# Optimization experiments

Measured on AMD Instinct MI355X. Metric: run time of the kernel, lower is better.

The kernel has to match this reference:

```python
import jax, jax.numpy as jnp
import numpy as np

P = 16      # patch size
DM = 512    # d_model
DI = 1024   # d_inner = expand * d_model
N = 16      # d_state
K = 4       # d_conv
DR = 32     # dt_rank = ceil(d_model/16)
NL = 8      # n_layers
NC = 1000   # num_classes


def _ln(x, w, b):
    m = x.mean(-1, keepdims=True)
    v = x.var(-1, keepdims=True)
    return (x - m) * jax.lax.rsqrt(v + 1e-5) * w + b


def _fpad(x, wl, wr, ht, hb):
    # torch F.pad(x, (wl, wr, ht, hb)) with possibly negative (crop) values, NCHW
    x = jnp.pad(x, ((0, 0), (0, 0), (max(ht, 0), max(hb, 0)), (max(wl, 0), max(wr, 0))))
    return x[:, :, -min(ht, 0):x.shape[2] + min(hb, 0), -min(wl, 0):x.shape[3] + min(wr, 0)]


def _mamba(x, in_w, conv_w, conv_b, xproj_w, dt_w, dt_b, A_log, Dp, out_w):
    # standard mamba_ssm Mamba layer; weights stored (in, out)
    B, L, _ = x.shape
    xz = x @ in_w                         # (B, L, 2*DI)
    xpart, z = xz[..., :DI], xz[..., DI:]
    # depthwise causal conv1d, kernel K, padding K-1 then truncate to L
    xc = jnp.pad(xpart.transpose(0, 2, 1), ((0, 0), (0, 0), (K - 1, 0)))  # (B, DI, L+K-1)
    conv = conv_b[None, :, None] + sum(conv_w[None, :, k, None] * xc[:, :, k:k + L] for k in range(K))
    u = jax.nn.silu(conv).transpose(0, 2, 1)    # (B, L, DI)
    dbc = u @ xproj_w                           # (B, L, DR + 2N)
    dt = jax.nn.softplus(dbc[..., :DR] @ dt_w + dt_b)  # (B, L, DI)
    Bm, Cm = dbc[..., DR:DR + N], dbc[..., DR + N:]
    A = -jnp.exp(A_log)                         # (DI, N)
    dA = jnp.exp(dt[..., None] * A)             # (B, L, DI, N)
    dBu = (dt * u)[..., None] * Bm[:, :, None, :]

    def step(h, inp):
        dA_t, dBu_t, C_t = inp
        h = dA_t * h + dBu_t                    # (B, DI, N)
        return h, jnp.einsum('bdn,bn->bd', h, C_t)

    h0 = jnp.zeros((B, DI, N), x.dtype)
    _, ys = jax.lax.scan(step, h0, (dA.transpose(1, 0, 2, 3), dBu.transpose(1, 0, 2, 3), Cm.transpose(1, 0, 2)))
    y = ys.transpose(1, 0, 2) + u * Dp          # (B, L, DI)
    return (y * jax.nn.silu(z)) @ out_w         # (B, L, DM)


def reference(img, patch_ln_w, patch_ln_b, patch_w, patch_b, pos_emb, cls_tok,
              ln_w, ln_b, in_w, conv_w, conv_b, xproj_w, dt_w, dt_b, A_log, D, out_w,
              head_ln_w, head_ln_b, head_w, head_b):
    shifts = ((1, -1, 0, 0), (-1, 1, 0, 0), (0, 0, 1, -1), (0, 0, -1, 1))
    x5 = jnp.concatenate([img] + [_fpad(img, *s) for s in shifts], axis=1)  # (B, 15, H, W)
    Bn, C, H, W = x5.shape
    # 'b c (h p1) (w p2) -> b (h w) (p1 p2 c)'
    x = x5.reshape(Bn, C, H // P, P, W // P, P).transpose(0, 2, 4, 3, 5, 1).reshape(Bn, (H // P) * (W // P), P * P * C)
    x = _ln(x, patch_ln_w, patch_ln_b) @ patch_w + patch_b  # (B, n, DM)
    n = x.shape[1]
    x = jnp.concatenate([x, jnp.broadcast_to(cls_tok, (Bn, 1, DM))], axis=1)  # cls appended at END
    x = x + pos_emb[:, :n + 1]
    for i in range(NL):
        y = _ln(x, ln_w[i], ln_b[i])
        x = x + _mamba(y, in_w[i], conv_w[i], conv_b[i], xproj_w[i], dt_w[i], dt_b[i], A_log[i], D[i], out_w[i])
    x = x[:, -1]  # pool='cls' -> last token
    return _ln(x, head_ln_w, head_ln_b) @ head_w + head_b


def setup_inputs() -> dict:
    key = jax.random.key(0)
    ks = jax.random.split(key, 12)
    B = 8
    PD = P * P * 15  # 3840
    rn = lambda k, shape, scale=1.0: jax.random.normal(k, shape, jnp.float32) * scale
    return {
        "img": rn(ks[0], (B, 3, 224, 224)),
        "patch_ln_w": jnp.ones((PD,), jnp.float32), "patch_ln_b": jnp.zeros((PD,), jnp.float32),
        "patch_w": rn(ks[1], (PD, DM), PD ** -0.5), "patch_b": jnp.zeros((DM,), jnp.float32),
        "pos_emb": rn(ks[2], (1, 197, DM), 0.02),
        "cls_tok": rn(ks[3], (1, 1, DM), 0.02),
        "ln_w": jnp.ones((NL, DM), jnp.float32), "ln_b": jnp.zeros((NL, DM), jnp.float32),
        "in_w": rn(ks[4], (NL, DM, 2 * DI), DM ** -0.5),
        "conv_w": rn(ks[5], (NL, DI, K), K ** -0.5),
        "conv_b": jnp.zeros((NL, DI), jnp.float32),
        "xproj_w": rn(ks[6], (NL, DI, DR + 2 * N), DI ** -0.5),
        "dt_w": rn(ks[7], (NL, DR, DI), DR ** -0.5),
        "dt_b": rn(ks[8], (NL, DI), 0.1) - 4.0,  # softplus -> small positive dt
        "A_log": jnp.log(jnp.broadcast_to(jnp.arange(1.0, N + 1.0, dtype=jnp.float32), (NL, DI, N))),
        "D": jnp.ones((NL, DI), jnp.float32),
        "out_w": rn(ks[9], (NL, DI, DM), DI ** -0.5),
        "head_ln_w": jnp.ones((DM,), jnp.float32), "head_ln_b": jnp.zeros((DM,), jnp.float32),
        "head_w": rn(ks[10], (DM, NC), DM ** -0.5), "head_b": jnp.zeros((NC,), jnp.float32),
    }
```

## Files before the change

kernel.cpp:

```cpp
#include <hip/hip_runtime.h>
#include <hip/hip_fp16.h>
#include <math.h>

#define BATCH   8
#define LSEQ    197
#define LPAD    200
#define NPATCH  196
#define NPTOK   (BATCH * NPATCH)
#define NTOK    (BATCH * LSEQ)
#define MPAD    1664
#define DMODEL  512
#define DINNER  1024
#define NSTATE  16
#define DRANK   32
#define NLAYER  8
#define NCLS    1000
#define PDIM    3840

typedef _Float16 f16x8 __attribute__((ext_vector_type(8)));
typedef float    f32x4 __attribute__((ext_vector_type(4)));
typedef unsigned short us8 __attribute__((ext_vector_type(8)));

__device__ __forceinline__ float f_rcp(float x) { return __builtin_amdgcn_rcpf(x); }
__device__ __forceinline__ float sp_silu(float x) { return x * f_rcp(1.0f + __expf(-x)); }
__device__ __forceinline__ float sp_softplus(float x) {
    return x > 20.0f ? x : __logf(1.0f + __expf(x));
}

template <int N>
__device__ __forceinline__ void vm_wait() {
    if constexpr (N == 0) asm volatile("s_waitcnt vmcnt(0)" ::: "memory");
    else if constexpr (N == 4) asm volatile("s_waitcnt vmcnt(4)" ::: "memory");
    else if constexpr (N == 6) asm volatile("s_waitcnt vmcnt(6)" ::: "memory");
    else if constexpr (N == 8) asm volatile("s_waitcnt vmcnt(8)" ::: "memory");
}

#define DPP_ROW_SHR_STEP(P, NB, CTRL)                                          \
    {                                                                          \
        float t_[NB];                                                          \
        _Pragma("unroll")                                                      \
        for (int i_ = 0; i_ < NB; ++i_)                                        \
            t_[i_] = __int_as_float(__builtin_amdgcn_update_dpp(               \
                0, __float_as_int(P[i_]), CTRL, 0xF, 0xF, true));              \
        _Pragma("unroll")                                                      \
        for (int i_ = 0; i_ < NB; ++i_) P[i_] += t_[i_];                       \
    }

template <int NB>
__device__ __forceinline__ void row_sum16v(float* p) {
    DPP_ROW_SHR_STEP(p, NB, 0x111);
    DPP_ROW_SHR_STEP(p, NB, 0x112);
    DPP_ROW_SHR_STEP(p, NB, 0x114);
    DPP_ROW_SHR_STEP(p, NB, 0x118);
}

__device__ __forceinline__ void store_f16(char* __restrict__ Hb,
                                          int row, int k, int K, float v) {
    size_t byte = (size_t)row * (size_t)(K * 2) +
                  (size_t)(((unsigned)(k * 2)) ^ (unsigned)((row & 7) << 4));
    *(__half*)(Hb + byte) = __float2half_rn(v);
}

__device__ __forceinline__ void store_f16x4(char* __restrict__ Hb,
                                            int row, int k4, int K, float4 v) {
    size_t byte = (size_t)row * (size_t)(K * 2) +
                  (size_t)(((unsigned)(k4 * 2)) ^ (unsigned)((row & 7) << 4));
    *(ushort4*)(Hb + byte) = make_ushort4(
        __half_as_ushort(__float2half_rn(v.x)), __half_as_ushort(__float2half_rn(v.y)),
        __half_as_ushort(__float2half_rn(v.z)), __half_as_ushort(__float2half_rn(v.w)));
}

__device__ __forceinline__ float2 block_reduce2(float a, float b, float* lds) {
#pragma unroll
    for (int off = 32; off > 0; off >>= 1) {
        a += __shfl_down(a, off);
        b += __shfl_down(b, off);
    }
    int lane = threadIdx.x & 63, w = threadIdx.x >> 6;
    if (lane == 0) { lds[w] = a; lds[4 + w] = b; }
    __syncthreads();
    float sa = lds[0] + lds[1] + lds[2] + lds[3];
    float sb = lds[4] + lds[5] + lds[6] + lds[7];
    return make_float2(sa, sb);
}

__global__ __launch_bounds__(256) void k_patch_ln(
    const float* __restrict__ img, const float* __restrict__ lnw,
    const float* __restrict__ lnb, char* __restrict__ Xph) {
    __shared__ float vals[PDIM];
    __shared__ float red[8];
    int tok = blockIdx.x;
    int b = tok / NPATCH, p = tok % NPATCH;
    int gy = p / 14, gx = p % 14;
    int tid = threadIdx.x;
    int py = tid >> 4, px = tid & 15;
    int h0 = gy * 16 + py, w0 = gx * 16 + px;
    const int dh[5] = {0, 0, 0, -1, 1};
    const int dw[5] = {0, -1, 1, 0, 0};
    float s = 0.f, ss = 0.f;
#pragma unroll
    for (int c = 0; c < 15; ++c) {
        int g = c / 3, ch = c % 3;
        int h = h0 + dh[g], w = w0 + dw[g];
        float v = 0.f;
        if ((unsigned)h < 224u && (unsigned)w < 224u)
            v = img[((b * 3 + ch) * 224 + h) * 224 + w];
        vals[tid * 15 + c] = v;
        s += v; ss += v * v;
    }
    float2 t2 = block_reduce2(s, ss, red);
    float mean = t2.x * (1.0f / PDIM);
    float var  = t2.y * (1.0f / PDIM) - mean * mean;
    float rstd = 1.0f / sqrtf(var + 1e-5f);
    for (int j = 0; j < 15; ++j) {
        int e = tid + j * 256;
        float v = (vals[e] - mean) * rstd * lnw[e] + lnb[e];
        store_f16(Xph, tok, e, PDIM, v);
    }
}

__global__ __launch_bounds__(256) void k_ln(
    const float* __restrict__ x, const float* __restrict__ w,
    const float* __restrict__ b, char* __restrict__ yh) {
    __shared__ float red[8];
    int t = blockIdx.x, tid = threadIdx.x;
    const float* xr = x + (size_t)t * DMODEL;
    float v0 = xr[tid], v1 = xr[tid + 256];
    float2 t2 = block_reduce2(v0 + v1, v0 * v0 + v1 * v1, red);
    float mean = t2.x * (1.0f / DMODEL);
    float var  = t2.y * (1.0f / DMODEL) - mean * mean;
    float rstd = 1.0f / sqrtf(var + 1e-5f);
    store_f16(yh, t, tid,       DMODEL, (v0 - mean) * rstd * w[tid]       + b[tid]);
    store_f16(yh, t, tid + 256, DMODEL, (v1 - mean) * rstd * w[tid + 256] + b[tid + 256]);
}

__global__ __launch_bounds__(256) void k_red_ln(
    const float* __restrict__ part, float* __restrict__ xtok,
    const float* __restrict__ w, const float* __restrict__ b,
    char* __restrict__ yh) {
    __shared__ float red[8];
    int t = blockIdx.x, tid = threadIdx.x;
    size_t base = (size_t)t * DMODEL;
    float v0 = xtok[base + tid], v1 = xtok[base + tid + 256];
#pragma unroll
    for (int k = 0; k < 4; ++k) {
        v0 += part[(size_t)k * (NTOK * DMODEL) + base + tid];
        v1 += part[(size_t)k * (NTOK * DMODEL) + base + tid + 256];
    }
    xtok[base + tid] = v0;
    xtok[base + tid + 256] = v1;
    float2 t2 = block_reduce2(v0 + v1, v0 * v0 + v1 * v1, red);
    float mean = t2.x * (1.0f / DMODEL);
    float var  = t2.y * (1.0f / DMODEL) - mean * mean;
    float rstd = 1.0f / sqrtf(var + 1e-5f);
    store_f16(yh, t, tid,       DMODEL, (v0 - mean) * rstd * w[tid]       + b[tid]);
    store_f16(yh, t, tid + 256, DMODEL, (v1 - mean) * rstd * w[tid + 256] + b[tid + 256]);
}

__global__ __launch_bounds__(256) void k_wT(
    const float* __restrict__ W, char* __restrict__ Th,
    int Ks, int Ns, size_t wStride, size_t tByteStride) {
    __shared__ float t[32][33];
    int z = blockIdx.z;
    const float* Wz = W + (size_t)z * wStride;
    char* ThZ = Th + (size_t)z * tByteStride;
    int n0 = blockIdx.x * 32, k0 = blockIdx.y * 32;
    int tx = threadIdx.x, ty = threadIdx.y;
#pragma unroll
    for (int r = 0; r < 4; ++r) {
        int k = k0 + ty + r * 8, n = n0 + tx;
        t[tx][ty + r * 8] = (n < Ns) ? Wz[(size_t)k * Ns + n] : 0.f;
    }
    __syncthreads();
#pragma unroll
    for (int r = 0; r < 4; ++r) {
        int n = n0 + ty + r * 8, k = k0 + tx;
        float v = t[ty + r * 8][tx];
        size_t byte = (size_t)n * (size_t)(Ks * 2) +
                      (size_t)(((unsigned)(k * 2)) ^ (unsigned)((n & 7) << 4));
        *(__half*)(ThZ + byte) = __float2half_rn(v);
    }
}

template <int TM, int TN, bool F16OUT>
__global__ __launch_bounds__(256, 3) void k_gemm(
    const char* __restrict__ Ah, const char* __restrict__ Bh,
    float* __restrict__ C, unsigned short* __restrict__ C16,
    int M, int N, int K, int kchunk, long partStride) {
    constexpr int MW = TM / 2, NW = TN / 2;
    constexpr int FM = MW / 16, FN = NW / 16;
    constexpr int CPW = (TM + TN) / 32;
    __shared__ __half L[2][(TM + TN) * 64];
    const int tid = threadIdx.x, w = tid >> 6, lane = tid & 63;

    const int GX = gridDim.x, GY = gridDim.y;
    const int nwg = GX * GY * gridDim.z;
    const int orig = blockIdx.x + GX * (blockIdx.y + GY * blockIdx.z);
    const int q = nwg >> 3, r = nwg & 7, xcd = orig & 7, pos = orig >> 3;
    const int wrk = (xcd < r ? xcd * (q + 1) : r * (q + 1) + (xcd - r) * q) + pos;
    const int bm = wrk % GY;
    const int t1 = wrk / GY;
    const int bn = t1 % GX, bz = t1 / GX;

    const int m0 = bm * TM, n0 = bn * TN;
    const int kbeg = bz * kchunk;
    int kend = kbeg + kchunk; if (kend > K) kend = K;
    C += (size_t)bz * (size_t)partStride;
    const size_t K2 = (size_t)K * 2;
    const int srLane = lane >> 3;
    const int scol = (lane & 7) * 16;

    f32x4 acc[FM][FN];
#pragma unroll
    for (int i = 0; i < FM; ++i)
#pragma unroll
        for (int j = 0; j < FN; ++j) acc[i][j] = (f32x4)(0.f);

    auto STAGE = [&](int buf, int k0) {
#pragma unroll
        for (int i = 0; i < CPW; ++i) {
            int cid = w * CPW + i;
            bool isA = cid < TM / 8;
            int lr = (isA ? cid : cid - TM / 8) * 8;
            size_t go = (size_t)((isA ? m0 : n0) + lr + srLane) * K2 +
                        (size_t)k0 * 2 + scol;
            const char* src = isA ? Ah : Bh;
            int ldsOff = (isA ? 0 : TM * 64) + lr * 64;
            __builtin_amdgcn_global_load_lds(
                (const __attribute__((address_space(1))) void*)(src + go),
                (__attribute__((address_space(3))) void*)&L[buf][ldsOff], 16, 0, 0);
        }
    };

    const int wm = w >> 1, wn = w & 1;
    const int g = lane >> 4, rr = lane & 15;
    const int nk = (kend - kbeg + 63) / 64;

    STAGE(0, kbeg);

    for (int t = 0; t < nk; ++t) {
        int cur = t & 1;
        if (t + 1 < nk) {
            STAGE(cur ^ 1, kbeg + (t + 1) * 64);
            vm_wait<CPW>();
        } else {
            vm_wait<0>();
        }
        __builtin_amdgcn_s_barrier();
        const char* Lb = (const char*)L[cur];
#pragma unroll
        for (int kk = 0; kk < 2; ++kk) {
            f16x8 af[FM], bf[FN];
#pragma unroll
            for (int mf = 0; mf < FM; ++mf) {
                int row = wm * MW + mf * 16 + rr;
                int off = row * 128 + ((kk * 64 + g * 16) ^ ((row & 7) << 4));
                af[mf] = *(const f16x8*)(Lb + off);
            }
#pragma unroll
            for (int nf = 0; nf < FN; ++nf) {
                int row = wn * NW + nf * 16 + rr;
                int off = TM * 128 + row * 128 +
                          ((kk * 64 + g * 16) ^ ((row & 7) << 4));
                bf[nf] = *(const f16x8*)(Lb + off);
            }
#pragma unroll
            for (int mf = 0; mf < FM; ++mf)
#pragma unroll
                for (int nf = 0; nf < FN; ++nf)
                    acc[mf][nf] = __builtin_amdgcn_mfma_f32_16x16x32_f16(
                        af[mf], bf[nf], acc[mf][nf], 0, 0, 0);
        }
        __builtin_amdgcn_s_barrier();
    }

#pragma unroll
    for (int mf = 0; mf < FM; ++mf)
#pragma unroll
        for (int nf = 0; nf < FN; ++nf)
#pragma unroll
            for (int e = 0; e < 4; ++e) {
                int gm = m0 + wm * MW + mf * 16 + g * 4 + e;
                int gn = n0 + wn * NW + nf * 16 + rr;
                if (gm < M && gn < N) {
                    if (F16OUT)
                        C16[(size_t)gm * N + gn] =
                            __half_as_ushort(__float2half_rn(acc[mf][nf][e]));
                    else
                        C[(size_t)gm * N + gn] = acc[mf][nf][e];
                }
            }
}

template <int SK, bool ACC>
__global__ __launch_bounds__(256) void k_reduce(
    const float* __restrict__ part, float* __restrict__ out, int total, int stride) {
    int i = blockIdx.x * 256 + threadIdx.x;
    if (i >= total) return;
    float s = 0.f;
#pragma unroll
    for (int k = 0; k < SK; ++k) s += part[(size_t)k * stride + i];
    out[i] = ACC ? out[i] + s : s;
}

__global__ __launch_bounds__(256) void k_assemble(
    const float* __restrict__ Pe, const float* __restrict__ patch_b,
    const float* __restrict__ cls, const float* __restrict__ pos,
    float* __restrict__ xtok) {
    int idx = blockIdx.x * 256 + threadIdx.x;
    if (idx >= NTOK * DMODEL) return;
    int d = idx % DMODEL;
    int t = (idx / DMODEL) % LSEQ;
    int b = idx / (DMODEL * LSEQ);
    float v = (t < NPATCH) ? (Pe[((size_t)b * NPATCH + t) * DMODEL + d] + patch_b[d])
                           : cls[d];
    xtok[idx] = v + pos[t * DMODEL + d];
}

__global__ __launch_bounds__(256) void k_conv(
    const unsigned short* __restrict__ xzH, const float* __restrict__ cw,
    const float* __restrict__ cb, char* __restrict__ uh) {
    int idx = blockIdx.x * 256 + threadIdx.x;
    if (idx >= NTOK * (DINNER / 4)) return;
    int dq = idx & (DINNER / 4 - 1);
    int t  = idx / (DINNER / 4);
    int l  = t % LSEQ;
    int d  = dq * 4;
    float4 w0 = *(const float4*)&cw[(d + 0) * 4];
    float4 w1 = *(const float4*)&cw[(d + 1) * 4];
    float4 w2 = *(const float4*)&cw[(d + 2) * 4];
    float4 w3 = *(const float4*)&cw[(d + 3) * 4];
    float4 acc = *(const float4*)&cb[d];
#pragma unroll
    for (int j = 0; j < 4; ++j) {
        int ls = l - 3 + j;
        if (ls >= 0) {
            union { ushort4 v; __half h[4]; } xu;
            xu.v = *(const ushort4*)&xzH[(size_t)(t - 3 + j) * (2 * DINNER) + d];
            acc.x += (&w0.x)[j] * __half2float(xu.h[0]);
            acc.y += (&w1.x)[j] * __half2float(xu.h[1]);
            acc.z += (&w2.x)[j] * __half2float(xu.h[2]);
            acc.w += (&w3.x)[j] * __half2float(xu.h[3]);
        }
    }
    float4 uv = make_float4(sp_silu(acc.x), sp_silu(acc.y),
                            sp_silu(acc.z), sp_silu(acc.w));
    store_f16x4(uh, t, d, DINNER, uv);
}

__global__ __launch_bounds__(256) void k_scan2(
    const char* __restrict__ uH, const float* __restrict__ dbc,
    const float* __restrict__ dtw, const float* __restrict__ dtb,
    const float* __restrict__ Alog, const float* __restrict__ Dp,
    const unsigned short* __restrict__ xzH, char* __restrict__ gh) {
    __shared__ float uS[LPAD * 16];
    __shared__ float dS[LPAD * 16];
    __shared__ float bS[LPAD * 16];
    __shared__ float cS[LPAD * 16];
    __shared__ float wS[DRANK * 16];
    const int tid = threadIdx.x;
    const int b = blockIdx.y, d0 = blockIdx.x * 16;

    for (int i = tid; i < DRANK * 16; i += 256)
        wS[i] = dtw[(size_t)(i >> 4) * DINNER + d0 + (i & 15)];
    __syncthreads();

    for (int i = tid; i < LPAD * 2; i += 256) {
        int l = i >> 1, jj = i & 1;
        float* dst = &uS[l * 16 + jj * 8];
        if (l >= LSEQ) {
#pragma unroll
            for (int e = 0; e < 8; ++e) dst[e] = 0.f;
            continue;
        }
        int t = b * LSEQ + l;
        size_t byte = (size_t)t * (DINNER * 2) +
                      (size_t)(((unsigned)(d0 * 2 + jj * 16)) ^ (unsigned)((t & 7) << 4));
        union { us8 v; __half h[8]; } uu;
        uu.v = *(const us8*)(uH + byte);
#pragma unroll
        for (int e = 0; e < 8; ++e) dst[e] = __half2float(uu.h[e]);
    }

    const float* dbcB = dbc + ((size_t)b * LSEQ) * 64;
    for (int i = tid; i < LPAD * 4; i += 256) {
        int l = i >> 2, j = (i & 3) << 2;
        if (l >= LSEQ) {
            float4 z = make_float4(0.f, 0.f, 0.f, 0.f);
            *(float4*)&dS[l * 16 + j] = z;
            *(float4*)&bS[l * 16 + j] = z;
            *(float4*)&cS[l * 16 + j] = z;
            continue;
        }
        *(float4*)&bS[l * 16 + j] = *(const float4*)&dbcB[(size_t)l * 64 + DRANK + j];
        *(float4*)&cS[l * 16 + j] = *(const float4*)&dbcB[(size_t)l * 64 + DRANK + 16 + j];
        float4 acc = *(const float4*)&dtb[d0 + j];
#pragma unroll
        for (int kq = 0; kq < DRANK / 4; ++kq) {
            float4 r4 = *(const float4*)&dbcB[(size_t)l * 64 + kq * 4];
#pragma unroll
            for (int m = 0; m < 4; ++m) {
                float rv = (&r4.x)[m];
                float4 w4 = *(const float4*)&wS[(kq * 4 + m) * 16 + j];
                acc.x += rv * w4.x; acc.y += rv * w4.y;
                acc.z += rv * w4.z; acc.w += rv * w4.w;
            }
        }
        dS[l * 16 + j + 0] = sp_softplus(acc.x);
        dS[l * 16 + j + 1] = sp_softplus(acc.y);
        dS[l * 16 + j + 2] = sp_softplus(acc.z);
        dS[l * 16 + j + 3] = sp_softplus(acc.w);
    }
    const int n = tid & 15, dsub = tid >> 4;
    const int d = d0 + dsub;
    const float A  = -__expf(Alog[d * NSTATE + n]);
    const float Dv = Dp[d];
    __syncthreads();

    float hn = 0.f;
    float dtc[8], uvc[8], Bnc[8], Cnc[8];
#pragma unroll
    for (int i = 0; i < 8; ++i) {
        int o = i * 16;
        dtc[i] = dS[o + dsub]; uvc[i] = uS[o + dsub];
        Bnc[i] = bS[o + n];    Cnc[i] = cS[o + n];
    }
    for (int lb = 0; lb < LPAD; lb += 8) {
        float dtN[8], uvN[8], BnN[8], CnN[8];
        if (lb + 8 < LPAD) {
#pragma unroll
            for (int i = 0; i < 8; ++i) {
                int o = (lb + 8 + i) * 16;
                dtN[i] = dS[o + dsub]; uvN[i] = uS[o + dsub];
                BnN[i] = bS[o + n];    CnN[i] = cS[o + n];
            }
        } else {
#pragma unroll
            for (int i = 0; i < 8; ++i) { dtN[i] = uvN[i] = BnN[i] = CnN[i] = 0.f; }
        }
        float a8[8], b8[8], p8[8];
#pragma unroll
        for (int i = 0; i < 8; ++i) {
            a8[i] = __expf(dtc[i] * A);
            b8[i] = dtc[i] * uvc[i] * Bnc[i];
        }
#pragma unroll
        for (int i = 0; i < 8; ++i) {
            hn = a8[i] * hn + b8[i];
            p8[i] = hn * Cnc[i];
        }
        row_sum16v<8>(p8);
#pragma unroll
        for (int i = 0; i < 8; ++i)
            if (n == 15) dS[(lb + i) * 16 + dsub] = p8[i] + uvc[i] * Dv;
#pragma unroll
        for (int i = 0; i < 8; ++i) {
            dtc[i] = dtN[i]; uvc[i] = uvN[i]; Bnc[i] = BnN[i]; Cnc[i] = CnN[i];
        }
    }
    __syncthreads();

    for (int i = tid; i < LSEQ * 4; i += 256) {
        int l = i >> 2, j = (i & 3) << 2;
        int t = b * LSEQ + l;
        union { ushort4 v; __half h[4]; } zu;
        zu.v = *(const ushort4*)&xzH[(size_t)t * (2 * DINNER) + DINNER + d0 + j];
        float4 g4 = make_float4(
            dS[l * 16 + j + 0] * sp_silu(__half2float(zu.h[0])),
            dS[l * 16 + j + 1] * sp_silu(__half2float(zu.h[1])),
            dS[l * 16 + j + 2] * sp_silu(__half2float(zu.h[2])),
            dS[l * 16 + j + 3] * sp_silu(__half2float(zu.h[3])));
        store_f16x4(gh, t, d0 + j, DINNER, g4);
    }
}

__global__ __launch_bounds__(256) void k_head_ln(
    const float* __restrict__ part, const float* __restrict__ xtok,
    const float* __restrict__ lnw, const float* __restrict__ lnb,
    float* __restrict__ xr) {
    __shared__ float red[8];
    int b = blockIdx.x, tid = threadIdx.x;
    size_t base = ((size_t)(b * LSEQ + NPATCH)) * DMODEL;
    float v0 = xtok[base + tid], v1 = xtok[base + tid + 256];
#pragma unroll
    for (int k = 0; k < 4; ++k) {
        v0 += part[(size_t)k * (NTOK * DMODEL) + base + tid];
        v1 += part[(size_t)k * (NTOK * DMODEL) + base + tid + 256];
    }
    float2 t2 = block_reduce2(v0 + v1, v0 * v0 + v1 * v1, red);
    float mean = t2.x * (1.0f / DMODEL);
    float var  = t2.y * (1.0f / DMODEL) - mean * mean;
    float rstd = 1.0f / sqrtf(var + 1e-5f);
    xr[b * DMODEL + tid]       = (v0 - mean) * rstd * lnw[tid] + lnb[tid];
    xr[b * DMODEL + tid + 256] = (v1 - mean) * rstd * lnw[tid + 256] + lnb[tid + 256];
}

__global__ __launch_bounds__(256) void k_head_fc(
    const float* __restrict__ xr, const float* __restrict__ hw,
    float* __restrict__ hpart) {
    __shared__ float xs[64];
    int tid = threadIdx.x;
    int c = blockIdx.x * 256 + tid;
    int b = blockIdx.y, ks = blockIdx.z;
    if (tid < 64) xs[tid] = xr[b * DMODEL + ks * 64 + tid];
    __syncthreads();
    if (c >= NCLS) return;
    float acc = 0.f;
#pragma unroll 8
    for (int k = 0; k < 64; ++k) acc += xs[k] * hw[(size_t)(ks * 64 + k) * NCLS + c];
    hpart[(size_t)(ks * BATCH + b) * NCLS + c] = acc;
}

__global__ __launch_bounds__(256) void k_head_red(
    const float* __restrict__ hpart, const float* __restrict__ hb,
    float* __restrict__ out) {
    int i = blockIdx.x * 256 + threadIdx.x;
    if (i >= BATCH * NCLS) return;
    int b = i / NCLS, c = i % NCLS;
    float s = hb[c];
#pragma unroll
    for (int ks = 0; ks < 8; ++ks) s += hpart[(size_t)(ks * BATCH + b) * NCLS + c];
    out[i] = s;
}

extern "C" void kernel_launch(void* const* d_in, const int* in_sizes, int n_in,
                              void* d_out, int out_size, void* d_ws, size_t ws_size,
                              hipStream_t stream) {
    const float* img     = (const float*)d_in[0];
    const float* plnw    = (const float*)d_in[1];
    const float* plnb    = (const float*)d_in[2];
    const float* patch_w = (const float*)d_in[3];
    const float* patch_b = (const float*)d_in[4];
    const float* pos     = (const float*)d_in[5];
    const float* cls     = (const float*)d_in[6];
    const float* ln_w    = (const float*)d_in[7];
    const float* ln_b    = (const float*)d_in[8];
    const float* in_w    = (const float*)d_in[9];
    const float* conv_w  = (const float*)d_in[10];
    const float* conv_b  = (const float*)d_in[11];
    const float* xproj   = (const float*)d_in[12];
    const float* dt_w    = (const float*)d_in[13];
    const float* dt_b    = (const float*)d_in[14];
    const float* A_log   = (const float*)d_in[15];
    const float* Dp      = (const float*)d_in[16];
    const float* out_w   = (const float*)d_in[17];
    const float* hlnw    = (const float*)d_in[18];
    const float* hlnb    = (const float*)d_in[19];
    const float* head_w  = (const float*)d_in[20];
    const float* head_b  = (const float*)d_in[21];
    float* out = (float*)d_out;

    char* p = (char*)d_ws;
    auto alloc = [&](size_t bytes) { char* r = p; p += (bytes + 255) & ~(size_t)255; return r; };
    float* xtok = (float*)alloc((size_t)NTOK * DMODEL * 4);
    unsigned short* xzH = (unsigned short*)alloc((size_t)NTOK * 2 * DINNER * 2);
    float* dbc  = (float*)alloc((size_t)NTOK * 64 * 4);
    float* Pe   = (float*)alloc((size_t)NPTOK * DMODEL * 4);
    float* part = (float*)alloc((size_t)4 * NTOK * DMODEL * 4);
    float* xr   = (float*)alloc((size_t)BATCH * DMODEL * 4);
    float* hpart= (float*)alloc((size_t)8 * BATCH * NCLS * 4);
    char* ylnH = alloc((size_t)MPAD * DMODEL * 2);
    char* uH   = alloc((size_t)MPAD * DINNER * 2);
    char* gH   = alloc((size_t)MPAD * DINNER * 2);
    char* XpH  = alloc((size_t)MPAD * PDIM * 2);
    char* inTH  = alloc((size_t)NLAYER * 2 * DINNER * DMODEL * 2);
    char* outTH = alloc((size_t)NLAYER * DMODEL * DINNER * 2);
    char* patTH = alloc((size_t)DMODEL * PDIM * 2);
    char* xprTH = alloc((size_t)NLAYER * 128 * DINNER * 2);

    const size_t IN_T_B  = (size_t)2 * DINNER * DMODEL * 2;
    const size_t OUT_T_B = (size_t)DMODEL * DINNER * 2;
    const size_t XPR_T_B = (size_t)128 * DINNER * 2;

    k_wT<<<dim3(2 * DINNER / 32, DMODEL / 32, NLAYER), dim3(32, 8), 0, stream>>>(
        in_w, inTH, DMODEL, 2 * DINNER, (size_t)DMODEL * 2 * DINNER, IN_T_B);
    k_wT<<<dim3(DMODEL / 32, DINNER / 32, NLAYER), dim3(32, 8), 0, stream>>>(
        out_w, outTH, DINNER, DMODEL, (size_t)DINNER * DMODEL, OUT_T_B);
    k_wT<<<dim3(DMODEL / 32, PDIM / 32, 1), dim3(32, 8), 0, stream>>>(
        patch_w, patTH, PDIM, DMODEL, 0, 0);
    k_wT<<<dim3(128 / 32, DINNER / 32, NLAYER), dim3(32, 8), 0, stream>>>(
        xproj, xprTH, DINNER, 64, (size_t)DINNER * 64, XPR_T_B);

    k_patch_ln<<<NPTOK, 256, 0, stream>>>(img, plnw, plnb, XpH);
    k_gemm<64, 128, false><<<dim3(4, 25, 4), 256, 0, stream>>>(
        XpH, patTH, part, nullptr, NPTOK, DMODEL, PDIM, 960, (long)NPTOK * DMODEL);
    k_reduce<4, false><<<(NPTOK * DMODEL + 255) / 256, 256, 0, stream>>>(
        part, Pe, NPTOK * DMODEL, NPTOK * DMODEL);
    k_assemble<<<(NTOK * DMODEL + 255) / 256, 256, 0, stream>>>(Pe, patch_b, cls, pos, xtok);

    for (int i = 0; i < NLAYER; ++i) {
        if (i == 0) {
            k_ln<<<NTOK, 256, 0, stream>>>(xtok, ln_w, ln_b, ylnH);
        } else {
            k_red_ln<<<NTOK, 256, 0, stream>>>(part, xtok, ln_w + i * DMODEL,
                                               ln_b + i * DMODEL, ylnH);
        }
        k_gemm<64, 128, true><<<dim3(16, 25, 1), 256, 0, stream>>>(
            ylnH, inTH + i * IN_T_B, nullptr, xzH, NTOK, 2 * DINNER, DMODEL, DMODEL, 0);
        k_conv<<<(NTOK * (DINNER / 4) + 255) / 256, 256, 0, stream>>>(
            xzH, conv_w + (size_t)i * DINNER * 4, conv_b + (size_t)i * DINNER, uH);
        k_gemm<64, 64, false><<<dim3(1, 25, 8), 256, 0, stream>>>(
            uH, xprTH + i * XPR_T_B, part, nullptr, NTOK, 64, DINNER, 128, (long)NTOK * 64);
        k_reduce<8, false><<<(NTOK * 64 + 255) / 256, 256, 0, stream>>>(
            part, dbc, NTOK * 64, NTOK * 64);
        k_scan2<<<dim3(DINNER / 16, BATCH), 256, 0, stream>>>(
            uH, dbc, dt_w + (size_t)i * DRANK * DINNER, dt_b + (size_t)i * DINNER,
            A_log + (size_t)i * DINNER * NSTATE, Dp + (size_t)i * DINNER,
            xzH, gH);
        k_gemm<64, 128, false><<<dim3(4, 25, 4), 256, 0, stream>>>(
            gH, outTH + i * OUT_T_B, part, nullptr, NTOK, DMODEL, DINNER, 256,
            (long)NTOK * DMODEL);
    }

    k_head_ln<<<BATCH, 256, 0, stream>>>(part, xtok, hlnw, hlnb, xr);
    k_head_fc<<<dim3(4, BATCH, 8), 256, 0, stream>>>(xr, head_w, hpart);
    k_head_red<<<(BATCH * NCLS + 255) / 256, 256, 0, stream>>>(hpart, head_b, out);
}
```

Before: 547.6 us.

## Triple-buffer GEMM staging, fuse patch reduce, reduce split-K, prefetch gate in scan

```diff
diff --git a/kernel.cpp b/kernel.cpp
--- a/kernel.cpp
+++ b/kernel.cpp
@@ -29,10 +29,11 @@
 
 template <int N>
 __device__ __forceinline__ void vm_wait() {
-    if constexpr (N == 0) asm volatile("s_waitcnt vmcnt(0)" ::: "memory");
-    else if constexpr (N == 4) asm volatile("s_waitcnt vmcnt(4)" ::: "memory");
-    else if constexpr (N == 6) asm volatile("s_waitcnt vmcnt(6)" ::: "memory");
-    else if constexpr (N == 8) asm volatile("s_waitcnt vmcnt(8)" ::: "memory");
+    if constexpr (N == 0)       asm volatile("s_waitcnt vmcnt(0)" ::: "memory");
+    else if constexpr (N == 4)  asm volatile("s_waitcnt vmcnt(4)" ::: "memory");
+    else if constexpr (N == 6)  asm volatile("s_waitcnt vmcnt(6)" ::: "memory");
+    else if constexpr (N == 8)  asm volatile("s_waitcnt vmcnt(8)" ::: "memory");
+    else if constexpr (N == 12) asm volatile("s_waitcnt vmcnt(12)" ::: "memory");
 }
 
 #define DPP_ROW_SHR_STEP(P, NB, CTRL)                                          \
@@ -143,7 +144,7 @@
     size_t base = (size_t)t * DMODEL;
     float v0 = xtok[base + tid], v1 = xtok[base + tid + 256];
 #pragma unroll
-    for (int k = 0; k < 4; ++k) {
+    for (int k = 0; k < 2; ++k) {
         v0 += part[(size_t)k * (NTOK * DMODEL) + base + tid];
         v1 += part[(size_t)k * (NTOK * DMODEL) + base + tid + 256];
     }
@@ -183,14 +184,14 @@
 }
 
 template <int TM, int TN, bool F16OUT>
-__global__ __launch_bounds__(256, 3) void k_gemm(
+__global__ __launch_bounds__(256, 2) void k_gemm(
     const char* __restrict__ Ah, const char* __restrict__ Bh,
     float* __restrict__ C, unsigned short* __restrict__ C16,
     int M, int N, int K, int kchunk, long partStride) {
     constexpr int MW = TM / 2, NW = TN / 2;
     constexpr int FM = MW / 16, FN = NW / 16;
     constexpr int CPW = (TM + TN) / 32;
-    __shared__ __half L[2][(TM + TN) * 64];
+    __shared__ __half L[3][(TM + TN) * 64];
     const int tid = threadIdx.x, w = tid >> 6, lane = tid & 63;
 
     const int GX = gridDim.x, GY = gridDim.y;
@@ -237,17 +238,19 @@
     const int nk = (kend - kbeg + 63) / 64;
 
     STAGE(0, kbeg);
+    if (1 < nk) STAGE(1, kbeg + 64);
 
     for (int t = 0; t < nk; ++t) {
-        int cur = t & 1;
-        if (t + 1 < nk) {
-            STAGE(cur ^ 1, kbeg + (t + 1) * 64);
+        if (t + 2 < nk) {
+            STAGE((t + 2) % 3, kbeg + (t + 2) * 64);
+            vm_wait<2 * CPW>();
+        } else if (t + 1 < nk) {
             vm_wait<CPW>();
         } else {
             vm_wait<0>();
         }
         __builtin_amdgcn_s_barrier();
-        const char* Lb = (const char*)L[cur];
+        const char* Lb = (const char*)L[t % 3];
 #pragma unroll
         for (int kk = 0; kk < 2; ++kk) {
             f16x8 af[FM], bf[FN];
@@ -303,8 +306,8 @@
     out[i] = ACC ? out[i] + s : s;
 }
 
-__global__ __launch_bounds__(256) void k_assemble(
-    const float* __restrict__ Pe, const float* __restrict__ patch_b,
+__global__ __launch_bounds__(256) void k_patch_asm(
+    const float* __restrict__ part, const float* __restrict__ patch_b,
     const float* __restrict__ cls, const float* __restrict__ pos,
     float* __restrict__ xtok) {
     int idx = blockIdx.x * 256 + threadIdx.x;
@@ -312,8 +315,16 @@
     int d = idx % DMODEL;
     int t = (idx / DMODEL) % LSEQ;
     int b = idx / (DMODEL * LSEQ);
-    float v = (t < NPATCH) ? (Pe[((size_t)b * NPATCH + t) * DMODEL + d] + patch_b[d])
-                           : cls[d];
+    float v;
+    if (t < NPATCH) {
+        size_t pi = ((size_t)(b * NPATCH + t)) * DMODEL + d;
+        float s = patch_b[d];
+#pragma unroll
+        for (int k = 0; k < 4; ++k) s += part[(size_t)k * (NPTOK * DMODEL) + pi];
+        v = s;
+    } else {
+        v = cls[d];
+    }
     xtok[idx] = v + pos[t * DMODEL + d];
 }
 
@@ -415,6 +426,17 @@
     const int d = d0 + dsub;
     const float A  = -__expf(Alog[d * NSTATE + n]);
     const float Dv = Dp[d];
+
+    ushort4 zreg[4];
+#pragma unroll
+    for (int it = 0; it < 4; ++it) {
+        int i = tid + it * 256;
+        if (i < LSEQ * 4) {
+            int l = i >> 2, j = (i & 3) << 2;
+            int t = b * LSEQ + l;
+            zreg[it] = *(const ushort4*)&xzH[(size_t)t * (2 * DINNER) + DINNER + d0 + j];
+        }
+    }
     __syncthreads();
 
     float hn = 0.f;
@@ -460,17 +482,21 @@
     }
     __syncthreads();
 
-    for (int i = tid; i < LSEQ * 4; i += 256) {
-        int l = i >> 2, j = (i & 3) << 2;
-        int t = b * LSEQ + l;
-        union { ushort4 v; __half h[4]; } zu;
-        zu.v = *(const ushort4*)&xzH[(size_t)t * (2 * DINNER) + DINNER + d0 + j];
-        float4 g4 = make_float4(
-            dS[l * 16 + j + 0] * sp_silu(__half2float(zu.h[0])),
-            dS[l * 16 + j + 1] * sp_silu(__half2float(zu.h[1])),
-            dS[l * 16 + j + 2] * sp_silu(__half2float(zu.h[2])),
-            dS[l * 16 + j + 3] * sp_silu(__half2float(zu.h[3])));
-        store_f16x4(gh, t, d0 + j, DINNER, g4);
+#pragma unroll
+    for (int it = 0; it < 4; ++it) {
+        int i = tid + it * 256;
+        if (i < LSEQ * 4) {
+            int l = i >> 2, j = (i & 3) << 2;
+            int t = b * LSEQ + l;
+            union { ushort4 v; __half h[4]; } zu;
+            zu.v = zreg[it];
+            float4 g4 = make_float4(
+                dS[l * 16 + j + 0] * sp_silu(__half2float(zu.h[0])),
+                dS[l * 16 + j + 1] * sp_silu(__half2float(zu.h[1])),
+                dS[l * 16 + j + 2] * sp_silu(__half2float(zu.h[2])),
+                dS[l * 16 + j + 3] * sp_silu(__half2float(zu.h[3])));
+            store_f16x4(gh, t, d0 + j, DINNER, g4);
+        }
     }
 }
 
@@ -483,7 +509,7 @@
     size_t base = ((size_t)(b * LSEQ + NPATCH)) * DMODEL;
     float v0 = xtok[base + tid], v1 = xtok[base + tid + 256];
 #pragma unroll
-    for (int k = 0; k < 4; ++k) {
+    for (int k = 0; k < 2; ++k) {
         v0 += part[(size_t)k * (NTOK * DMODEL) + base + tid];
         v1 += part[(size_t)k * (NTOK * DMODEL) + base + tid + 256];
     }
@@ -555,7 +581,6 @@
     float* xtok = (float*)alloc((size_t)NTOK * DMODEL * 4);
     unsigned short* xzH = (unsigned short*)alloc((size_t)NTOK * 2 * DINNER * 2);
     float* dbc  = (float*)alloc((size_t)NTOK * 64 * 4);
-    float* Pe   = (float*)alloc((size_t)NPTOK * DMODEL * 4);
     float* part = (float*)alloc((size_t)4 * NTOK * DMODEL * 4);
     float* xr   = (float*)alloc((size_t)BATCH * DMODEL * 4);
     float* hpart= (float*)alloc((size_t)8 * BATCH * NCLS * 4);
@@ -584,9 +609,8 @@
     k_patch_ln<<<NPTOK, 256, 0, stream>>>(img, plnw, plnb, XpH);
     k_gemm<64, 128, false><<<dim3(4, 25, 4), 256, 0, stream>>>(
         XpH, patTH, part, nullptr, NPTOK, DMODEL, PDIM, 960, (long)NPTOK * DMODEL);
-    k_reduce<4, false><<<(NPTOK * DMODEL + 255) / 256, 256, 0, stream>>>(
-        part, Pe, NPTOK * DMODEL, NPTOK * DMODEL);
-    k_assemble<<<(NTOK * DMODEL + 255) / 256, 256, 0, stream>>>(Pe, patch_b, cls, pos, xtok);
+    k_patch_asm<<<(NTOK * DMODEL + 255) / 256, 256, 0, stream>>>(
+        part, patch_b, cls, pos, xtok);
 
     for (int i = 0; i < NLAYER; ++i) {
         if (i == 0) {
@@ -599,16 +623,16 @@
             ylnH, inTH + i * IN_T_B, nullptr, xzH, NTOK, 2 * DINNER, DMODEL, DMODEL, 0);
         k_conv<<<(NTOK * (DINNER / 4) + 255) / 256, 256, 0, stream>>>(
             xzH, conv_w + (size_t)i * DINNER * 4, conv_b + (size_t)i * DINNER, uH);
-        k_gemm<64, 64, false><<<dim3(1, 25, 8), 256, 0, stream>>>(
-            uH, xprTH + i * XPR_T_B, part, nullptr, NTOK, 64, DINNER, 128, (long)NTOK * 64);
-        k_reduce<8, false><<<(NTOK * 64 + 255) / 256, 256, 0, stream>>>(
+        k_gemm<64, 64, false><<<dim3(1, 25, 4), 256, 0, stream>>>(
+            uH, xprTH + i * XPR_T_B, part, nullptr, NTOK, 64, DINNER, 256, (long)NTOK * 64);
+        k_reduce<4, false><<<(NTOK * 64 + 255) / 256, 256, 0, stream>>>(
             part, dbc, NTOK * 64, NTOK * 64);
         k_scan2<<<dim3(DINNER / 16, BATCH), 256, 0, stream>>>(
             uH, dbc, dt_w + (size_t)i * DRANK * DINNER, dt_b + (size_t)i * DINNER,
             A_log + (size_t)i * DINNER * NSTATE, Dp + (size_t)i * DINNER,
             xzH, gH);
-        k_gemm<64, 128, false><<<dim3(4, 25, 4), 256, 0, stream>>>(
-            gH, outTH + i * OUT_T_B, part, nullptr, NTOK, DMODEL, DINNER, 256,
+        k_gemm<64, 128, false><<<dim3(4, 25, 2), 256, 0, stream>>>(
+            gH, outTH + i * OUT_T_B, part, nullptr, NTOK, DMODEL, DINNER, 512,
             (long)NTOK * DMODEL);
     }
 
```

Result: no change. 545.6 us (median of 2 runs) (-0.4%).
